# Kernel tuning notes

Measured on AMD Instinct MI355X. Metric: run time of the kernel, lower is better.

The kernel has to match this reference:

```python
import jax, jax.numpy as jnp
import numpy as np

H = 16        # num_attention_heads
HS = 128      # head_size
ROT = 32      # rotary_ndims (partial RoPE, NeoX rotary_pct=0.25)
BASE = 10000.0


def _rope_cache(seq_len):
    inv_freq = 1.0 / (BASE ** (jnp.arange(0, ROT, 2, dtype=jnp.float32) / ROT))
    t = jnp.arange(seq_len, dtype=jnp.float32)
    freqs = jnp.outer(t, inv_freq)                      # [s, ROT/2]
    emb = jnp.concatenate([freqs, freqs], axis=-1)      # [s, ROT]
    return jnp.cos(emb), jnp.sin(emb)


def _rotate_half(x):
    x1, x2 = jnp.split(x, 2, axis=-1)
    return jnp.concatenate([-x2, x1], axis=-1)


def setup_inputs() -> dict:
    key = jax.random.key(0)
    k1, k2, k3 = jax.random.split(key, 3)
    B, S, D = 2, 2048, 2048
    hidden_states = jax.random.normal(k1, (B, S, D), dtype=jnp.float32)
    position_ids = jnp.broadcast_to(jnp.arange(S, dtype=jnp.int64 if jax.config.jax_enable_x64 else jnp.int32), (B, S))
    W_qkv = jax.random.normal(k2, (D, 3 * H * HS), dtype=jnp.float32) * 0.02
    b_qkv = jnp.zeros((3 * H * HS,), dtype=jnp.float32)
    W_dense = jax.random.normal(k3, (H * HS, D), dtype=jnp.float32) * 0.02
    b_dense = jnp.zeros((D,), dtype=jnp.float32)
    return {"hidden_states": hidden_states, "position_ids": position_ids,
            "W_qkv": W_qkv, "b_qkv": b_qkv, "W_dense": W_dense, "b_dense": b_dense}


def reference(hidden_states, position_ids, W_qkv, b_qkv, W_dense, b_dense):
    B, S, D = hidden_states.shape
    # fused QKV projection, NeoX layout: [b, s, h, 3*hs]
    qkv = (hidden_states @ W_qkv + b_qkv).reshape(B, S, H, 3 * HS)
    q = qkv[..., :HS]            # [b, s, h, hs]
    k = qkv[..., HS:2 * HS]
    v = qkv[..., 2 * HS:]

    # partial rotary embedding on first ROT dims
    cos, sin = _rope_cache(S)                       # [s, ROT]
    cos = cos[position_ids][:, :, None, :]          # [b, s, 1, ROT]
    sin = sin[position_ids][:, :, None, :]
    q_rot, q_pass = q[..., :ROT], q[..., ROT:]
    k_rot, k_pass = k[..., :ROT], k[..., ROT:]
    q_rot = q_rot * cos + _rotate_half(q_rot) * sin
    k_rot = k_rot * cos + _rotate_half(k_rot) * sin
    q = jnp.concatenate([q_rot, q_pass], axis=-1)
    k = jnp.concatenate([k_rot, k_pass], axis=-1)

    # scaled dot-product attention (no mask, as in the source SDPA call)
    scale = 1.0 / jnp.sqrt(jnp.asarray(HS, dtype=q.dtype))
    scores = jnp.einsum('bqhd,bkhd->bhqk', q, k) * scale   # [b, h, s, s]
    attn = jax.nn.softmax(scores, axis=-1)
    out = jnp.einsum('bhqk,bkhd->bqhd', attn, v)            # [b, s, h, hs]
    out = out.reshape(B, S, H * HS)                         # 'b h d n -> b d (h n)'
    return out @ W_dense + b_dense
```

## Files before the change

### kernel.cpp

```cpp
#include <hip/hip_runtime.h>

typedef short bf16x8 __attribute__((ext_vector_type(8)));
typedef float f32x4 __attribute__((ext_vector_type(4)));

#define S_LEN 2048
#define NHEAD 16
#define HSZ 128

__device__ __forceinline__ float bf2f(ushort u) {
    union { unsigned int i; float f; } x; x.i = ((unsigned int)u) << 16; return x.f;
}
__device__ __forceinline__ ushort f2bf(float f) {
    union { float f; unsigned int i; } x; x.f = f;
    unsigned int r = (x.i + 0x7FFFu + ((x.i >> 16) & 1u)) >> 16;
    return (ushort)r;
}

__device__ __forceinline__ void gload16(const ushort* g, ushort* l) {
    __builtin_amdgcn_global_load_lds(
        (const __attribute__((address_space(1))) unsigned int*)g,
        (__attribute__((address_space(3))) unsigned int*)l,
        16, 0, 0);
}

#define BAR()   asm volatile("s_barrier" ::: "memory")
#define LGKM0() asm volatile("s_waitcnt lgkmcnt(0)" ::: "memory")

__global__ void cast_kernel(const float* __restrict__ in, ushort* __restrict__ out, int n4) {
    int i = blockIdx.x * 256 + threadIdx.x;
    if (i >= n4) return;
    float4 v = ((const float4*)in)[i];
    ushort4 r;
    r.x = f2bf(v.x); r.y = f2bf(v.y); r.z = f2bf(v.z); r.w = f2bf(v.w);
    ((ushort4*)out)[i] = r;
}

__global__ void transpose_cast(const float* __restrict__ W, ushort* __restrict__ WT,
                               int K, int N) {
    __shared__ float tile[32][33];
    int n = blockIdx.x * 32 + threadIdx.x;
    #pragma unroll
    for (int j = 0; j < 32; j += 8) {
        int k = blockIdx.y * 32 + threadIdx.y + j;
        tile[threadIdx.y + j][threadIdx.x] = W[(size_t)k * N + n];
    }
    __syncthreads();
    int k2 = blockIdx.y * 32 + threadIdx.x;
    #pragma unroll
    for (int j = 0; j < 32; j += 8) {
        int n2 = blockIdx.x * 32 + threadIdx.y + j;
        WT[(size_t)n2 * K + k2] = f2bf(tile[threadIdx.x][threadIdx.y + j]);
    }
}

template <int EPI>
__global__ __launch_bounds__(512, 2) void gemm256(
    const ushort* __restrict__ A, const ushort* __restrict__ Bt,
    const float* __restrict__ bias, float* __restrict__ Cout, int Kdim, int Ndim,
    ushort* __restrict__ q_out, ushort* __restrict__ k_out, ushort* __restrict__ v_out) {
    __shared__ __align__(16) ushort lds[65536];
    const int tid = threadIdx.x;
    const int m0 = blockIdx.y * 256, n0 = blockIdx.x * 256;
    const int lane = tid & 63, wid = tid >> 6;
    const int wm = wid >> 2, wn = wid & 3;
    const int lm = lane & 15, quad = lane >> 4;
    const int cs = (quad ^ ((lm >> 1) & 3)) * 8;
    const int aOff = wm * 8192 + lm * 32 + cs;
    const int bOff = 16384 + (wn >> 1) * 8192 + (wn & 1) * 2048 + lm * 32 + cs;
    const int srow = tid >> 2;
    const int xs8 = ((tid & 3) ^ ((tid >> 3) & 3)) * 8;
    const ushort* pAs = A  + (size_t)(m0 + srow) * Kdim + xs8;
    const ushort* pBs = Bt + (size_t)(n0 + srow) * Kdim + xs8;
    const size_t hK = (size_t)128 * Kdim;
    const int sw = wid * 512;

    f32x4 acc[8][4];
    #pragma unroll
    for (int i = 0; i < 8; ++i)
        #pragma unroll
        for (int j = 0; j < 4; ++j) acc[i][j] = (f32x4){0.f, 0.f, 0.f, 0.f};

    const int T = Kdim >> 6;

    auto stageB = [&](int t) {
        ushort* b = lds + (t & 1) * 32768 + 16384 + sw;
        const ushort* g = pBs + (size_t)t * 64;
        gload16(g,            b);
        gload16(g + 32,       b + 4096);
        gload16(g + hK,       b + 8192);
        gload16(g + hK + 32,  b + 12288);
    };
    auto stageA = [&](int t) {
        ushort* b = lds + (t & 1) * 32768 + sw;
        const ushort* g = pAs + (size_t)t * 64;
        gload16(g,            b);
        gload16(g + 32,       b + 4096);
        gload16(g + hK,       b + 8192);
        gload16(g + hK + 32,  b + 12288);
    };

    stageB(0); stageA(0); stageB(1); stageA(1);
    asm volatile("s_waitcnt vmcnt(8)" ::: "memory");
    BAR();

    for (int t = 0; t < T; ++t) {
        const ushort* la = lds + (t & 1) * 32768 + aOff;
        const ushort* lb = lds + (t & 1) * 32768 + bOff;
        const bool pf = (t + 2 < T);

        bf16x8 afL[4][2], bfL[2][2];
        #pragma unroll
        for (int mt = 0; mt < 4; ++mt)
            #pragma unroll
            for (int ks = 0; ks < 2; ++ks)
                afL[mt][ks] = *(const bf16x8*)(la + ks * 4096 + mt * 512);
        #pragma unroll
        for (int nt = 0; nt < 2; ++nt)
            #pragma unroll
            for (int ks = 0; ks < 2; ++ks)
                bfL[nt][ks] = *(const bf16x8*)(lb + ks * 4096 + nt * 512);
        BAR(); LGKM0();
        __builtin_amdgcn_s_setprio(1);
        #pragma unroll
        for (int mt = 0; mt < 4; ++mt)
            #pragma unroll
            for (int nt = 0; nt < 2; ++nt) {
                acc[mt][nt] = __builtin_amdgcn_mfma_f32_16x16x32_bf16(afL[mt][0], bfL[nt][0], acc[mt][nt], 0, 0, 0);
                acc[mt][nt] = __builtin_amdgcn_mfma_f32_16x16x32_bf16(afL[mt][1], bfL[nt][1], acc[mt][nt], 0, 0, 0);
            }
        __builtin_amdgcn_s_setprio(0);
        BAR();

        bf16x8 bfH[2][2];
        #pragma unroll
        for (int nt = 0; nt < 2; ++nt)
            #pragma unroll
            for (int ks = 0; ks < 2; ++ks)
                bfH[nt][ks] = *(const bf16x8*)(lb + ks * 4096 + (nt + 2) * 512);
        BAR(); LGKM0();
        __builtin_amdgcn_s_setprio(1);
        #pragma unroll
        for (int mt = 0; mt < 4; ++mt)
            #pragma unroll
            for (int nt = 0; nt < 2; ++nt) {
                acc[mt][nt + 2] = __builtin_amdgcn_mfma_f32_16x16x32_bf16(afL[mt][0], bfH[nt][0], acc[mt][nt + 2], 0, 0, 0);
                acc[mt][nt + 2] = __builtin_amdgcn_mfma_f32_16x16x32_bf16(afL[mt][1], bfH[nt][1], acc[mt][nt + 2], 0, 0, 0);
            }
        __builtin_amdgcn_s_setprio(0);
        BAR();

        bf16x8 afH[4][2];
        #pragma unroll
        for (int mt = 0; mt < 4; ++mt)
            #pragma unroll
            for (int ks = 0; ks < 2; ++ks)
                afH[mt][ks] = *(const bf16x8*)(la + ks * 4096 + (mt + 4) * 512);
        if (pf) stageB(t + 2);
        BAR(); LGKM0();
        __builtin_amdgcn_s_setprio(1);
        #pragma unroll
        for (int mt = 0; mt < 4; ++mt)
            #pragma unroll
            for (int nt = 0; nt < 2; ++nt) {
                acc[mt + 4][nt] = __builtin_amdgcn_mfma_f32_16x16x32_bf16(afH[mt][0], bfL[nt][0], acc[mt + 4][nt], 0, 0, 0);
                acc[mt + 4][nt] = __builtin_amdgcn_mfma_f32_16x16x32_bf16(afH[mt][1], bfL[nt][1], acc[mt + 4][nt], 0, 0, 0);
            }
        __builtin_amdgcn_s_setprio(0);
        BAR();

        if (pf) stageA(t + 2);
        BAR();
        __builtin_amdgcn_s_setprio(1);
        #pragma unroll
        for (int mt = 0; mt < 4; ++mt)
            #pragma unroll
            for (int nt = 0; nt < 2; ++nt) {
                acc[mt + 4][nt + 2] = __builtin_amdgcn_mfma_f32_16x16x32_bf16(afH[mt][0], bfH[nt][0], acc[mt + 4][nt + 2], 0, 0, 0);
                acc[mt + 4][nt + 2] = __builtin_amdgcn_mfma_f32_16x16x32_bf16(afH[mt][1], bfH[nt][1], acc[mt + 4][nt + 2], 0, 0, 0);
            }
        __builtin_amdgcn_s_setprio(0);
        if (pf) asm volatile("s_waitcnt vmcnt(8)" ::: "memory");
        else    asm volatile("s_waitcnt vmcnt(0)" ::: "memory");
        BAR();
    }

    #pragma unroll
    for (int mt = 0; mt < 8; ++mt) {
        #pragma unroll
        for (int nt = 0; nt < 4; ++nt) {
            f32x4 c = acc[mt][nt];
            int gn = n0 + wn * 64 + nt * 16 + lm;
            float bv = bias[gn];
            #pragma unroll
            for (int i = 0; i < 4; ++i) {
                int gm = m0 + wm * 128 + mt * 16 + quad * 4 + i;
                float v = c[i] + bv;
                if (EPI == 0) {
                    int h = gn / 384, r = gn - h * 384;
                    int tt = r >> 7, d = r & 127;
                    int b = gm >> 11, s = gm & 2047;
                    ushort bb = f2bf(v);
                    if (tt == 0) {
                        q_out[((size_t)(b * NHEAD + h) * S_LEN + s) * HSZ + d] = bb;
                    } else if (tt == 1) {
                        k_out[((size_t)(b * NHEAD + h) * S_LEN + s) * HSZ + d] = bb;
                    } else {
                        v_out[((size_t)(b * NHEAD + h) * HSZ + d) * S_LEN + s] = bb;
                    }
                } else {
                    Cout[(size_t)gm * Ndim + gn] = v;
                }
            }
        }
    }
}

template <int EPI>
__global__ __launch_bounds__(256) void gemm128(
    const ushort* __restrict__ A, const ushort* __restrict__ Bt,
    const float* __restrict__ bias, float* __restrict__ Cout, int Kdim, int Ndim,
    ushort* __restrict__ q_out, ushort* __restrict__ k_out, ushort* __restrict__ v_out) {
    __shared__ __align__(16) ushort lA[2][128 * 32];
    __shared__ __align__(16) ushort lB[2][128 * 32];
    const int tid = threadIdx.x;
    const int m0 = blockIdx.y * 128, n0 = blockIdx.x * 128;
    const int lane = tid & 63, wid = tid >> 6;
    const int wm = wid >> 1, wn = wid & 1, lm = lane & 15, quad = lane >> 4;
    const int srow = tid >> 2;
    const int gc = (tid & 3) ^ ((tid >> 3) & 3);
    const int wb8 = (wid << 6) * 8;
    const int cs = (quad ^ ((lm >> 1) & 3)) * 8;

    const ushort* pA = A  + (size_t)(m0 + srow) * Kdim + gc * 8;
    const ushort* pB = Bt + (size_t)(n0 + srow) * Kdim + gc * 8;
    const size_t rhalf = (size_t)64 * Kdim;

    const int fA = (wm * 64 + lm) * 32;
    const int fB = (wn * 64 + lm) * 32;

    f32x4 acc[16];
    #pragma unroll
    for (int i = 0; i < 16; ++i) acc[i] = (f32x4){0.f, 0.f, 0.f, 0.f};

    const int T = Kdim >> 5;
    gload16(pA,         lA[0] + wb8);
    gload16(pA + rhalf, lA[0] + 2048 + wb8);
    gload16(pB,         lB[0] + wb8);
    gload16(pB + rhalf, lB[0] + 2048 + wb8);
    pA += 32; pB += 32;

    for (int t = 0; t < T; ++t) {
        __syncthreads();
        const ushort* la = lA[t & 1];
        const ushort* lb = lB[t & 1];
        if (t + 1 < T) {
            ushort* da = lA[(t + 1) & 1];
            ushort* db = lB[(t + 1) & 1];
            gload16(pA,         da + wb8);
            gload16(pA + rhalf, da + 2048 + wb8);
            gload16(pB,         db + wb8);
            gload16(pB + rhalf, db + 2048 + wb8);
            pA += 32; pB += 32;
        }
        bf16x8 af[4], bfr[4];
        #pragma unroll
        for (int t4 = 0; t4 < 4; ++t4) {
            af[t4]  = *(const bf16x8*)(la + fA + t4 * 512 + cs);
            bfr[t4] = *(const bf16x8*)(lb + fB + t4 * 512 + cs);
        }
        #pragma unroll
        for (int mt = 0; mt < 4; ++mt)
            #pragma unroll
            for (int nt = 0; nt < 4; ++nt)
                acc[mt * 4 + nt] = __builtin_amdgcn_mfma_f32_16x16x32_bf16(
                    af[mt], bfr[nt], acc[mt * 4 + nt], 0, 0, 0);
    }

    #pragma unroll
    for (int mt = 0; mt < 4; ++mt) {
        #pragma unroll
        for (int nt = 0; nt < 4; ++nt) {
            f32x4 c = acc[mt * 4 + nt];
            int gn = n0 + wn * 64 + nt * 16 + lm;
            float bv = bias[gn];
            #pragma unroll
            for (int i = 0; i < 4; ++i) {
                int gm = m0 + wm * 64 + mt * 16 + quad * 4 + i;
                float v = c[i] + bv;
                if (EPI == 0) {
                    int h = gn / 384, r = gn - h * 384;
                    int t = r >> 7, d = r & 127;
                    int b = gm >> 11, s = gm & 2047;
                    ushort bb = f2bf(v);
                    if (t == 0) {
                        q_out[((size_t)(b * NHEAD + h) * S_LEN + s) * HSZ + d] = bb;
                    } else if (t == 1) {
                        k_out[((size_t)(b * NHEAD + h) * S_LEN + s) * HSZ + d] = bb;
                    } else {
                        v_out[((size_t)(b * NHEAD + h) * HSZ + d) * S_LEN + s] = bb;
                    }
                } else {
                    Cout[(size_t)gm * Ndim + gn] = v;
                }
            }
        }
    }
}

__global__ void rope_kernel(ushort* __restrict__ Qr, ushort* __restrict__ Kr,
                            const int* __restrict__ pos_ids) {
    int idx = blockIdx.x * 256 + threadIdx.x;
    int j = idx & 15;
    int row = idx >> 4;
    int s = row & 2047;
    int bh = row >> 11;
    int b = bh >> 4;
    int pos = pos_ids[b * S_LEN + s];
    float inv = exp2f((float)j * -0.8304820237218405f);
    float th = (float)pos * inv;
    float sn, c;
    sincosf(th, &sn, &c);
    size_t base = (size_t)row * HSZ;
    {
        float x1 = bf2f(Qr[base + j]), x2 = bf2f(Qr[base + j + 16]);
        Qr[base + j]      = f2bf(x1 * c - x2 * sn);
        Qr[base + j + 16] = f2bf(x2 * c + x1 * sn);
    }
    {
        float x1 = bf2f(Kr[base + j]), x2 = bf2f(Kr[base + j + 16]);
        Kr[base + j]      = f2bf(x1 * c - x2 * sn);
        Kr[base + j + 16] = f2bf(x2 * c + x1 * sn);
    }
}

__global__ __launch_bounds__(512, 2) void attn_mfma(
    const ushort* __restrict__ Q, const ushort* __restrict__ K,
    const ushort* __restrict__ Vt, ushort* __restrict__ O) {
    __shared__ __align__(16) ushort lQ[256 * 136];
    __shared__ __align__(16) ushort lK[2][64 * 128];
    __shared__ __align__(16) ushort lVt[2][128 * 64];
    __shared__ __align__(16) ushort lP[8 * 32 * 40];

    const int tid = threadIdx.x;
    const int wid = tid >> 6, lane = tid & 63;
    const int L = lane & 15, quad = lane >> 4;
    const int bh = blockIdx.y;
    const int q0 = blockIdx.x * 256;
    const int wq0 = wid * 32;
    const size_t base = (size_t)bh * S_LEN * HSZ;
    const ushort* Qb = Q + base + (size_t)q0 * HSZ;
    const ushort* Kb = K + base;
    const ushort* Vb = Vt + base;
    ushort* lPw = lP + wid * (32 * 40);

    #pragma unroll
    for (int p = 0; p < 8; ++p) {
        int idx = tid + p * 512;
        int row = idx >> 4, ch = idx & 15;
        uint4 v = ((const uint4*)Qb)[idx];
        *(uint4*)(lQ + row * 136 + ch * 8) = v;
    }
    __syncthreads();

    bf16x8 qf[2][4];
    #pragma unroll
    for (int qs = 0; qs < 2; ++qs)
        #pragma unroll
        for (int dc = 0; dc < 4; ++dc)
            qf[qs][dc] = *(const bf16x8*)(lQ + (wq0 + qs * 16 + L) * 136 + dc * 32 + quad * 8);

    int kx[4];
    #pragma unroll
    for (int dc = 0; dc < 4; ++dc) kx[dc] = ((dc * 4 + quad) ^ (L & 7)) * 8;
    const int vx0 = ((0 * 4 + quad) ^ (L & 7)) * 8;
    const int vx1 = ((1 * 4 + quad) ^ (L & 7)) * 8;

    const int ub  = (tid & 0x1C0) * 8;
    const int kr0 = tid >> 4,  kg0 = (tid & 15) ^ (kr0 & 7);
    const int kr1 = kr0 + 32;
    const int vd0 = tid >> 3,  vg0 = (tid & 7) ^ (vd0 & 7);
    const int vd1 = vd0 + 64;

    f32x4 acc_o[8][2];
    #pragma unroll
    for (int dt = 0; dt < 8; ++dt)
        #pragma unroll
        for (int qs = 0; qs < 2; ++qs) acc_o[dt][qs] = (f32x4){0.f, 0.f, 0.f, 0.f};
    float lacc[2] = {0.f, 0.f};
    const float scale = 0.08838834764831845f;
    const float SHIFT = 12.0f;

    {
        gload16(Kb + (size_t)kr0 * 128 + kg0 * 8, lK[0] + ub);
        gload16(Kb + (size_t)kr1 * 128 + kg0 * 8, lK[0] + 4096 + ub);
        gload16(Vb + (size_t)vd0 * 2048 + vg0 * 8, lVt[0] + ub);
        gload16(Vb + (size_t)vd1 * 2048 + vg0 * 8, lVt[0] + 4096 + ub);
    }

    for (int kt = 0; kt < S_LEN / 64; ++kt) {
        __syncthreads();
        const int cur = kt & 1;
        const ushort* lKc = lK[cur];
        const ushort* lVc = lVt[cur];
        if (kt + 1 < S_LEN / 64) {
            ushort* dK = lK[cur ^ 1];
            ushort* dV = lVt[cur ^ 1];
            int kb = (kt + 1) * 64;
            gload16(Kb + (size_t)(kb + kr0) * 128 + kg0 * 8, dK + ub);
            gload16(Kb + (size_t)(kb + kr1) * 128 + kg0 * 8, dK + 4096 + ub);
            gload16(Vb + (size_t)vd0 * 2048 + kb + vg0 * 8, dV + ub);
            gload16(Vb + (size_t)vd1 * 2048 + kb + vg0 * 8, dV + 4096 + ub);
        }

        f32x4 sa[4][2];
        #pragma unroll
        for (int t = 0; t < 4; ++t)
            #pragma unroll
            for (int qs = 0; qs < 2; ++qs) sa[t][qs] = (f32x4){0.f, 0.f, 0.f, 0.f};
        #pragma unroll
        for (int t = 0; t < 4; ++t)
            #pragma unroll
            for (int dc = 0; dc < 4; ++dc) {
                bf16x8 kf = *(const bf16x8*)(lKc + (t * 16 + L) * 128 + kx[dc]);
                sa[t][0] = __builtin_amdgcn_mfma_f32_16x16x32_bf16(kf, qf[0][dc], sa[t][0], 0, 0, 0);
                sa[t][1] = __builtin_amdgcn_mfma_f32_16x16x32_bf16(kf, qf[1][dc], sa[t][1], 0, 0, 0);
            }

        #pragma unroll
        for (int h = 0; h < 2; ++h) {
            #pragma unroll
            for (int t2 = 0; t2 < 2; ++t2) {
                int t = h * 2 + t2;
                #pragma unroll
                for (int qs = 0; qs < 2; ++qs) {
                    #pragma unroll
                    for (int r = 0; r < 4; ++r) {
                        float pv = __expf(fmaf(sa[t][qs][r], scale, -SHIFT));
                        lacc[qs] += pv;
                        sa[t][qs][r] = pv;
                    }
                    ushort4 u;
                    u.x = f2bf(sa[t][qs][0]);
                    u.y = f2bf(sa[t][qs][1]);
                    u.z = f2bf(sa[t][qs][2]);
                    u.w = f2bf(sa[t][qs][3]);
                    *(ushort4*)(lPw + (qs * 16 + L) * 40 + t2 * 16 + quad * 4) = u;
                }
            }
            LGKM0();
            bf16x8 pf0 = *(const bf16x8*)(lPw + L * 40 + quad * 8);
            bf16x8 pf1 = *(const bf16x8*)(lPw + (16 + L) * 40 + quad * 8);
            const int vx = h ? vx1 : vx0;
            #pragma unroll
            for (int dt = 0; dt < 8; ++dt) {
                bf16x8 vf = *(const bf16x8*)(lVc + (dt * 16 + L) * 64 + vx);
                acc_o[dt][0] = __builtin_amdgcn_mfma_f32_16x16x32_bf16(vf, pf0, acc_o[dt][0], 0, 0, 0);
                acc_o[dt][1] = __builtin_amdgcn_mfma_f32_16x16x32_bf16(vf, pf1, acc_o[dt][1], 0, 0, 0);
            }
        }
    }

    const int b = bh >> 4, h = bh & 15;
    #pragma unroll
    for (int qs = 0; qs < 2; ++qs) {
        float l = lacc[qs];
        l += __shfl_xor(l, 16);
        l += __shfl_xor(l, 32);
        float inv = 1.f / l;
        size_t row = ((size_t)(b * S_LEN + q0 + wq0 + qs * 16 + L)) * (NHEAD * HSZ) + h * HSZ;
        #pragma unroll
        for (int dt = 0; dt < 8; ++dt) {
            ushort4 u;
            u.x = f2bf(acc_o[dt][qs][0] * inv);
            u.y = f2bf(acc_o[dt][qs][1] * inv);
            u.z = f2bf(acc_o[dt][qs][2] * inv);
            u.w = f2bf(acc_o[dt][qs][3] * inv);
            *(ushort4*)(O + row + dt * 16 + quad * 4) = u;
        }
    }
}

extern "C" void kernel_launch(void* const* d_in, const int* in_sizes, int n_in,
                              void* d_out, int out_size, void* d_ws, size_t ws_size,
                              hipStream_t stream) {
    const float* hidden = (const float*)d_in[0];
    const int*   pos    = (const int*)d_in[1];
    const float* Wqkv   = (const float*)d_in[2];
    const float* bqkv   = (const float*)d_in[3];
    const float* Wd     = (const float*)d_in[4];
    const float* bd     = (const float*)d_in[5];

    char* ws = (char*)d_ws;
    ushort* hA  = (ushort*)ws;
    ushort* WqT = (ushort*)(ws + 16777216ull);
    ushort* WdT = (ushort*)(ws + 41943040ull);
    ushort* Qb  = (ushort*)(ws + 50331648ull);
    ushort* Kb  = (ushort*)(ws + 67108864ull);
    ushort* Vb  = (ushort*)(ws + 83886080ull);

    cast_kernel<<<dim3(8192), dim3(256), 0, stream>>>(hidden, hA, 2097152);
    transpose_cast<<<dim3(192, 64), dim3(32, 8), 0, stream>>>(Wqkv, WqT, 2048, 6144);
    transpose_cast<<<dim3(64, 64), dim3(32, 8), 0, stream>>>(Wd, WdT, 2048, 2048);

    gemm256<0><<<dim3(24, 16), dim3(512), 0, stream>>>(hA, WqT, bqkv, nullptr, 2048, 6144,
                                                       Qb, Kb, Vb);
    rope_kernel<<<dim3(4096), dim3(256), 0, stream>>>(Qb, Kb, pos);

    ushort* Obuf = hA;
    attn_mfma<<<dim3(8, 32), dim3(512), 0, stream>>>(Qb, Kb, Vb, Obuf);

    gemm128<1><<<dim3(16, 32), dim3(256), 0, stream>>>(Obuf, WdT, bd, (float*)d_out,
                                                       2048, 2048, nullptr, nullptr, nullptr);
}
```

Baseline: 431.7 us.

## Fuse prep kernels, fold RoPE into QKV GEMM epilogue, swizzle block order

Merges the cast and two transpose-cast kernels into one launch. Applies rotary embedding inside the QKV GEMM epilogue, so the separate RoPE kernel and its extra read and write of Q/K are gone. Remaps workgroup IDs in both GEMMs and the attention kernel, so that consecutive blocks are spread across the 8 XCDs in chunks and blocks on one XCD share L2-resident tiles. The trade-offs are more epilogue work (sincos per row), a rotation that depends on 64-column warp tiles lining up with head boundaries, and the loss of coalescing if the remap is wrong.

After: 431.2 us. About the same (-0.1%).

```diff
diff --git a/kernel.cpp b/kernel.cpp
--- a/kernel.cpp
+++ b/kernel.cpp
@@ -26,30 +26,43 @@
 #define BAR()   asm volatile("s_barrier" ::: "memory")
 #define LGKM0() asm volatile("s_waitcnt lgkmcnt(0)" ::: "memory")
 
-__global__ void cast_kernel(const float* __restrict__ in, ushort* __restrict__ out, int n4) {
-    int i = blockIdx.x * 256 + threadIdx.x;
-    if (i >= n4) return;
-    float4 v = ((const float4*)in)[i];
-    ushort4 r;
-    r.x = f2bf(v.x); r.y = f2bf(v.y); r.z = f2bf(v.z); r.w = f2bf(v.w);
-    ((ushort4*)out)[i] = r;
-}
-
-__global__ void transpose_cast(const float* __restrict__ W, ushort* __restrict__ WT,
-                               int K, int N) {
+__device__ __forceinline__ void transpose_body(
+    const float* __restrict__ W, ushort* __restrict__ WT,
+    int K, int N, int bx, int by, float (*tile)[33]) {
+    int tx = threadIdx.x & 31, ty = threadIdx.x >> 5;
+    int n = bx * 32 + tx;
+    #pragma unroll
+    for (int j = 0; j < 32; j += 8) {
+        int k = by * 32 + ty + j;
+        tile[ty + j][tx] = W[(size_t)k * N + n];
+    }
+    __syncthreads();
+    int k2 = by * 32 + tx;
+    #pragma unroll
+    for (int j = 0; j < 32; j += 8) {
+        int n2 = bx * 32 + ty + j;
+        WT[(size_t)n2 * K + k2] = f2bf(tile[tx][ty + j]);
+    }
+}
+
+__global__ __launch_bounds__(256) void prep_kernel(
+    const float* __restrict__ hidden, ushort* __restrict__ hA,
+    const float* __restrict__ Wqkv, ushort* __restrict__ WqT,
+    const float* __restrict__ Wd, ushort* __restrict__ WdT) {
     __shared__ float tile[32][33];
-    int n = blockIdx.x * 32 + threadIdx.x;
-    #pragma unroll
-    for (int j = 0; j < 32; j += 8) {
-        int k = blockIdx.y * 32 + threadIdx.y + j;
-        tile[threadIdx.y + j][threadIdx.x] = W[(size_t)k * N + n];
-    }
-    __syncthreads();
-    int k2 = blockIdx.y * 32 + threadIdx.x;
-    #pragma unroll
-    for (int j = 0; j < 32; j += 8) {
-        int n2 = blockIdx.x * 32 + threadIdx.y + j;
-        WT[(size_t)n2 * K + k2] = f2bf(tile[threadIdx.x][threadIdx.y + j]);
+    int bid = blockIdx.x;
+    if (bid < 8192) {
+        int i = bid * 256 + threadIdx.x;
+        float4 v = ((const float4*)hidden)[i];
+        ushort4 r;
+        r.x = f2bf(v.x); r.y = f2bf(v.y); r.z = f2bf(v.z); r.w = f2bf(v.w);
+        ((ushort4*)hA)[i] = r;
+    } else if (bid < 8192 + 12288) {
+        int tb = bid - 8192;
+        transpose_body(Wqkv, WqT, 2048, 6144, tb % 192, tb / 192, tile);
+    } else {
+        int tb = bid - 20480;
+        transpose_body(Wd, WdT, 2048, 2048, tb % 64, tb / 64, tile);
     }
 }
 
@@ -57,10 +70,16 @@
 __global__ __launch_bounds__(512, 2) void gemm256(
     const ushort* __restrict__ A, const ushort* __restrict__ Bt,
     const float* __restrict__ bias, float* __restrict__ Cout, int Kdim, int Ndim,
-    ushort* __restrict__ q_out, ushort* __restrict__ k_out, ushort* __restrict__ v_out) {
+    ushort* __restrict__ q_out, ushort* __restrict__ k_out, ushort* __restrict__ v_out,
+    const int* __restrict__ pos_ids) {
     __shared__ __align__(16) ushort lds[65536];
     const int tid = threadIdx.x;
-    const int m0 = blockIdx.y * 256, n0 = blockIdx.x * 256;
+    const int nwg = gridDim.x * gridDim.y;
+    const int bid0 = blockIdx.y * gridDim.x + blockIdx.x;
+    const int chunk = nwg >> 3;
+    const int swz = (bid0 & 7) * chunk + (bid0 >> 3);
+    const int bx = swz % gridDim.x, by = swz / gridDim.x;
+    const int m0 = by * 256, n0 = bx * 256;
     const int lane = tid & 63, wid = tid >> 6;
     const int wm = wid >> 2, wn = wid & 3;
     const int lm = lane & 15, quad = lane >> 4;
@@ -184,22 +203,44 @@
         BAR();
     }
 
-    #pragma unroll
-    for (int mt = 0; mt < 8; ++mt) {
-        #pragma unroll
-        for (int nt = 0; nt < 4; ++nt) {
-            f32x4 c = acc[mt][nt];
-            int gn = n0 + wn * 64 + nt * 16 + lm;
-            float bv = bias[gn];
-            #pragma unroll
-            for (int i = 0; i < 4; ++i) {
-                int gm = m0 + wm * 128 + mt * 16 + quad * 4 + i;
-                float v = c[i] + bv;
-                if (EPI == 0) {
-                    int h = gn / 384, r = gn - h * 384;
-                    int tt = r >> 7, d = r & 127;
+    if (EPI == 0) {
+        const int woff = (n0 + wn * 64) % 384;
+        const int rot = (woff == 0 || woff == 128) ? 1 : 0;
+        float invf = 0.f;
+        if (rot) invf = exp2f(-(float)lm * 0.8304820237218405f);
+        const int gnb = n0 + wn * 64 + lm;
+        #pragma unroll
+        for (int mt = 0; mt < 8; ++mt) {
+            f32x4 w[4];
+            #pragma unroll
+            for (int nt = 0; nt < 4; ++nt) {
+                float bv = bias[gnb + nt * 16];
+                #pragma unroll
+                for (int i = 0; i < 4; ++i) w[nt][i] = acc[mt][nt][i] + bv;
+            }
+            if (rot) {
+                #pragma unroll
+                for (int i = 0; i < 4; ++i) {
+                    int gm = m0 + wm * 128 + mt * 16 + quad * 4 + i;
+                    int bI = gm >> 11, s = gm & 2047;
+                    float th = (float)pos_ids[bI * S_LEN + s] * invf;
+                    float sf, cf;
+                    sincosf(th, &sf, &cf);
+                    float x1 = w[0][i], x2 = w[1][i];
+                    w[0][i] = x1 * cf - x2 * sf;
+                    w[1][i] = x2 * cf + x1 * sf;
+                }
+            }
+            #pragma unroll
+            for (int nt = 0; nt < 4; ++nt) {
+                int gn = gnb + nt * 16;
+                int h = gn / 384, r = gn - h * 384;
+                int tt = r >> 7, d = r & 127;
+                #pragma unroll
+                for (int i = 0; i < 4; ++i) {
+                    int gm = m0 + wm * 128 + mt * 16 + quad * 4 + i;
                     int b = gm >> 11, s = gm & 2047;
-                    ushort bb = f2bf(v);
+                    ushort bb = f2bf(w[nt][i]);
                     if (tt == 0) {
                         q_out[((size_t)(b * NHEAD + h) * S_LEN + s) * HSZ + d] = bb;
                     } else if (tt == 1) {
@@ -207,8 +248,21 @@
                     } else {
                         v_out[((size_t)(b * NHEAD + h) * HSZ + d) * S_LEN + s] = bb;
                     }
-                } else {
-                    Cout[(size_t)gm * Ndim + gn] = v;
+                }
+            }
+        }
+    } else {
+        #pragma unroll
+        for (int mt = 0; mt < 8; ++mt) {
+            #pragma unroll
+            for (int nt = 0; nt < 4; ++nt) {
+                f32x4 c = acc[mt][nt];
+                int gn = n0 + wn * 64 + nt * 16 + lm;
+                float bv = bias[gn];
+                #pragma unroll
+                for (int i = 0; i < 4; ++i) {
+                    int gm = m0 + wm * 128 + mt * 16 + quad * 4 + i;
+                    Cout[(size_t)gm * Ndim + gn] = c[i] + bv;
                 }
             }
         }
@@ -223,7 +277,12 @@
     __shared__ __align__(16) ushort lA[2][128 * 32];
     __shared__ __align__(16) ushort lB[2][128 * 32];
     const int tid = threadIdx.x;
-    const int m0 = blockIdx.y * 128, n0 = blockIdx.x * 128;
+    const int nwg = gridDim.x * gridDim.y;
+    const int bid0 = blockIdx.y * gridDim.x + blockIdx.x;
+    const int chunk = nwg >> 3;
+    const int swz = (bid0 & 7) * chunk + (bid0 >> 3);
+    const int bx = swz % gridDim.x, by = swz / gridDim.x;
+    const int m0 = by * 128, n0 = bx * 128;
     const int lane = tid & 63, wid = tid >> 6;
     const int wm = wid >> 1, wn = wid & 1, lm = lane & 15, quad = lane >> 4;
     const int srow = tid >> 2;
@@ -307,32 +366,6 @@
     }
 }
 
-__global__ void rope_kernel(ushort* __restrict__ Qr, ushort* __restrict__ Kr,
-                            const int* __restrict__ pos_ids) {
-    int idx = blockIdx.x * 256 + threadIdx.x;
-    int j = idx & 15;
-    int row = idx >> 4;
-    int s = row & 2047;
-    int bh = row >> 11;
-    int b = bh >> 4;
-    int pos = pos_ids[b * S_LEN + s];
-    float inv = exp2f((float)j * -0.8304820237218405f);
-    float th = (float)pos * inv;
-    float sn, c;
-    sincosf(th, &sn, &c);
-    size_t base = (size_t)row * HSZ;
-    {
-        float x1 = bf2f(Qr[base + j]), x2 = bf2f(Qr[base + j + 16]);
-        Qr[base + j]      = f2bf(x1 * c - x2 * sn);
-        Qr[base + j + 16] = f2bf(x2 * c + x1 * sn);
-    }
-    {
-        float x1 = bf2f(Kr[base + j]), x2 = bf2f(Kr[base + j + 16]);
-        Kr[base + j]      = f2bf(x1 * c - x2 * sn);
-        Kr[base + j + 16] = f2bf(x2 * c + x1 * sn);
-    }
-}
-
 __global__ __launch_bounds__(512, 2) void attn_mfma(
     const ushort* __restrict__ Q, const ushort* __restrict__ K,
     const ushort* __restrict__ Vt, ushort* __restrict__ O) {
@@ -344,8 +377,10 @@
     const int tid = threadIdx.x;
     const int wid = tid >> 6, lane = tid & 63;
     const int L = lane & 15, quad = lane >> 4;
-    const int bh = blockIdx.y;
-    const int q0 = blockIdx.x * 256;
+    const int bid0 = blockIdx.y * 8 + blockIdx.x;
+    const int swz = (bid0 & 7) * 32 + (bid0 >> 3);
+    const int bh = swz >> 3;
+    const int q0 = (swz & 7) * 256;
     const int wq0 = wid * 32;
     const size_t base = (size_t)bh * S_LEN * HSZ;
     const ushort* Qb = Q + base + (size_t)q0 * HSZ;
@@ -498,13 +533,10 @@
     ushort* Kb  = (ushort*)(ws + 67108864ull);
     ushort* Vb  = (ushort*)(ws + 83886080ull);
 
-    cast_kernel<<<dim3(8192), dim3(256), 0, stream>>>(hidden, hA, 2097152);
-    transpose_cast<<<dim3(192, 64), dim3(32, 8), 0, stream>>>(Wqkv, WqT, 2048, 6144);
-    transpose_cast<<<dim3(64, 64), dim3(32, 8), 0, stream>>>(Wd, WdT, 2048, 2048);
+    prep_kernel<<<dim3(24576), dim3(256), 0, stream>>>(hidden, hA, Wqkv, WqT, Wd, WdT);
 
     gemm256<0><<<dim3(24, 16), dim3(512), 0, stream>>>(hA, WqT, bqkv, nullptr, 2048, 6144,
-                                                       Qb, Kb, Vb);
-    rope_kernel<<<dim3(4096), dim3(256), 0, stream>>>(Qb, Kb, pos);
+                                                       Qb, Kb, Vb, pos);
 
     ushort* Obuf = hA;
     attn_mfma<<<dim3(8, 32), dim3(512), 0, stream>>>(Qb, Kb, Vb, Obuf);
```
